# Optimization experiments

Hardware: AMD Instinct MI355X
Metric: run time of the kernel (lower is better)

The kernel has to match this reference:

```python
import jax, jax.numpy as jnp
import numpy as np

N_EXPERTS = 8
TOP_K = 2
C = 2048       # n_embd
H = 1024       # expert_intermediate_size
HS = 2048      # shared_expert_intermediate_size
B, T = 1, 512
SCALE = 0.02


def setup_inputs() -> dict:
    key = jax.random.key(0)
    ks = jax.random.split(key, 10)
    x = jax.random.normal(ks[0], (B, T, C), dtype=jnp.float32)
    gate_w = jax.random.normal(ks[1], (N_EXPERTS, C), dtype=jnp.float32) * SCALE
    w_gate = jax.random.normal(ks[2], (N_EXPERTS, H, C), dtype=jnp.float32) * SCALE
    w_up = jax.random.normal(ks[3], (N_EXPERTS, H, C), dtype=jnp.float32) * SCALE
    w_down = jax.random.normal(ks[4], (N_EXPERTS, C, H), dtype=jnp.float32) * SCALE
    sh_gate = jax.random.normal(ks[5], (HS, C), dtype=jnp.float32) * SCALE
    sh_up = jax.random.normal(ks[6], (HS, C), dtype=jnp.float32) * SCALE
    sh_down = jax.random.normal(ks[7], (C, HS), dtype=jnp.float32) * SCALE
    se_gate_w = jax.random.normal(ks[8], (1, C), dtype=jnp.float32) * SCALE
    return {"x": x, "gate_w": gate_w, "w_gate": w_gate, "w_up": w_up,
            "w_down": w_down, "sh_gate": sh_gate, "sh_up": sh_up,
            "sh_down": sh_down, "se_gate_w": se_gate_w}


def reference(x, gate_w, w_gate, w_up, w_down, sh_gate, sh_up, sh_down, se_gate_w):
    Bb, Tt, Cc = x.shape
    xf = x.reshape(-1, Cc)                      # (t, d)
    # routing
    scores = xf @ gate_w.T                      # (t, E)
    ew, ei = jax.lax.top_k(scores, TOP_K)       # (t, A)
    ew = jax.nn.softmax(ew, axis=-1)
    # expert FFN (dense over experts; identical math to per-token gathered einsum)
    x1 = jax.nn.silu(jnp.einsum('td,ehd->teh', xf, w_gate))
    x3 = jnp.einsum('td,ehd->teh', xf, w_up)
    expert_out = jnp.einsum('teh,edh->ted', x1 * x3, w_down)  # (t, E, d)
    # combine: routed[t] = sum_a ew[t,a] * expert_out[t, ei[t,a]]
    onehot = jax.nn.one_hot(ei, N_EXPERTS, dtype=ew.dtype)    # (t, A, E)
    comb = jnp.einsum('ta,tae->te', ew, onehot)               # (t, E)
    routed = jnp.einsum('te,ted->td', comb, expert_out)
    # shared expert (SwiGLU MLP)
    shared = (jax.nn.silu(xf @ sh_gate.T) * (xf @ sh_up.T)) @ sh_down.T
    sgate = jax.nn.sigmoid(xf @ se_gate_w.T)                  # (t, 1)
    return (routed + sgate * shared).reshape(Bb, Tt, Cc)
```

## Files before the change

### kernel.cpp

```cpp
#include <hip/hip_runtime.h>

typedef unsigned short u16;
typedef u16 u16x8 __attribute__((ext_vector_type(8)));
typedef __bf16 bf16x8 __attribute__((ext_vector_type(8)));
typedef float f32x4 __attribute__((ext_vector_type(4)));

#define NE 8

__device__ __forceinline__ unsigned pk2(float a, float b) {
  unsigned ua = __builtin_bit_cast(unsigned, a) + 0x8000u;
  unsigned ub = __builtin_bit_cast(unsigned, b) + 0x8000u;
  return __builtin_amdgcn_perm(ub, ua, 0x07060302);
}
__device__ __forceinline__ u16 f2bf(float f) {
  return (u16)((__builtin_bit_cast(unsigned, f) + 0x8000u) >> 16);
}
__device__ __forceinline__ bf16x8 ldfrag(const u16* p) {
  union { u16x8 u; bf16x8 b; } x;
  x.u = *(const u16x8*)p;
  return x.b;
}
__device__ __forceinline__ void gld16(const void* g, void* l) {
  __builtin_amdgcn_global_load_lds(
      (const __attribute__((address_space(1))) unsigned int*)g,
      (__attribute__((address_space(3))) unsigned int*)l, 16, 0, 0);
}
#define MFMA16 __builtin_amdgcn_mfma_f32_16x16x32_bf16

__global__ __launch_bounds__(64) void route_prep_kernel(
    const float* __restrict__ x, const float* __restrict__ gw,
    const float* __restrict__ segw, int* __restrict__ counts,
    int* __restrict__ ptok, float* __restrict__ pw, float* __restrict__ sgate,
    u16* __restrict__ xb) {
  int t = blockIdx.x;
  int lane = threadIdx.x;
  const float* xr = x + (size_t)t * 2048;
  u16* xbr = xb + (size_t)t * 2048;
  float s[NE];
#pragma unroll
  for (int e = 0; e < NE; e++) s[e] = 0.f;
  float sg = 0.f;
#pragma unroll
  for (int it = 0; it < 8; it++) {
    int c = it * 256 + lane * 4;
    f32x4 xv = *(const f32x4*)(xr + c);
    *(uint2*)(xbr + c) = make_uint2(pk2(xv[0], xv[1]), pk2(xv[2], xv[3]));
#pragma unroll
    for (int e = 0; e < NE; e++) {
      f32x4 wv4 = *(const f32x4*)(gw + e * 2048 + c);
      s[e] += xv[0] * wv4[0] + xv[1] * wv4[1] + xv[2] * wv4[2] + xv[3] * wv4[3];
    }
    f32x4 sv = *(const f32x4*)(segw + c);
    sg += xv[0] * sv[0] + xv[1] * sv[1] + xv[2] * sv[2] + xv[3] * sv[3];
  }
#pragma unroll
  for (int off = 32; off > 0; off >>= 1) {
#pragma unroll
    for (int e = 0; e < NE; e++) s[e] += __shfl_down(s[e], off);
    sg += __shfl_down(sg, off);
  }
  if (lane == 0) {
    int i0 = 0;
#pragma unroll
    for (int e = 1; e < NE; e++) if (s[e] > s[i0]) i0 = e;
    int i1 = (i0 == 0) ? 1 : 0;
#pragma unroll
    for (int e = 0; e < NE; e++) if (e != i0 && s[e] > s[i1]) i1 = e;
    float r = __expf(s[i1] - s[i0]);
    float w0 = 1.f / (1.f + r);
    float w1 = 1.f - w0;
    int s0 = atomicAdd(&counts[i0], 1);
    ptok[(i0 << 9) + s0] = t; pw[(i0 << 9) + s0] = w0;
    int s1 = atomicAdd(&counts[i1], 1);
    ptok[(i1 << 9) + s1] = t; pw[(i1 << 9) + s1] = w1;
    sgate[t] = 1.f / (1.f + __expf(-sg));
  }
}

__global__ __launch_bounds__(256) void gateup_kernel(
    const u16* __restrict__ xb, const float* __restrict__ Wg,
    const float* __restrict__ Wu, const float* __restrict__ SWg,
    const float* __restrict__ SWu, u16* __restrict__ hbufB,
    u16* __restrict__ hsB, const int* __restrict__ ptok,
    const int* __restrict__ counts) {
  __shared__ __align__(16) u16 As[3 * 8192];
  __shared__ __align__(16) u16 Bs[3 * 4096];

  int b = blockIdx.x;
  int t = threadIdx.x;
  int is_ex = (b < 1024);
  int e = 0, j, mt, cnt;
  const float *gW, *uW;
  u16* obase;
  if (is_ex) {
    e = b & 7; j = (b >> 3) & 31; mt = b >> 8;
    cnt = counts[e];
    if (mt * 128 >= cnt) return;
    gW = Wg + (size_t)(e * 1024 + j * 32) * 2048;
    uW = Wu + (size_t)(e * 1024 + j * 32) * 2048;
    obase = hbufB + (size_t)(e * 64 + 2 * j) * 8192;
  } else {
    int bs = b - 1024;
    int xcd = bs & 7; mt = (bs >> 3) & 3; j = (bs >> 5) * 8 + xcd; cnt = 512;
    gW = SWg + (size_t)(j * 32) * 2048;
    uW = SWu + (size_t)(j * 32) * 2048;
    obase = hsB + (size_t)(2 * j) * 8192;
  }

  int lane = t & 63, wv = t >> 6;
  int quad = lane >> 4, l16 = lane & 15;

  const u16* aptr[4];
  int aoff[4];
#pragma unroll
  for (int i = 0; i < 4; i++) {
    int c = 4 * wv + i;
    int row = 8 * c + (lane >> 3);
    int slot = mt * 128 + row;
    int tok = is_ex ? ((slot < cnt) ? ptok[(e << 9) + slot] : 0) : slot;
    aptr[i] = xb + (size_t)tok * 2048 + (((lane & 7) ^ ((lane >> 3) & 7)) * 8);
    aoff[i] = c * 512;
  }
  const float* bsrc[4];
  int bwr[4];
#pragma unroll
  for (int i = 0; i < 4; i++) {
    int rloc = wv * 16 + i * 4 + quad;
    const float* base = (rloc < 32) ? (gW + (size_t)rloc * 2048)
                                    : (uW + (size_t)(rloc - 32) * 2048);
    bsrc[i] = base + l16 * 4;
    bwr[i] = rloc * 64 + (((l16 >> 1) ^ (rloc & 7)) * 8) + ((l16 & 1) * 4);
  }

  f32x4 bA0, bA1, bA2, bA3, bB0, bB1, bB2, bB3;
  f32x4 acc00 = {}, acc01 = {}, acc02 = {}, acc03 = {};
  f32x4 acc10 = {}, acc11 = {}, acc12 = {}, acc13 = {};

#define GU_ISSUE(kt1, ao, S)                                                \
  S##0 = *(const f32x4*)(bsrc[0] + (kt1) * 64);                             \
  S##1 = *(const f32x4*)(bsrc[1] + (kt1) * 64);                             \
  S##2 = *(const f32x4*)(bsrc[2] + (kt1) * 64);                             \
  S##3 = *(const f32x4*)(bsrc[3] + (kt1) * 64);                             \
  gld16(aptr[0] + (kt1) * 64, &As[(ao) + aoff[0]]);                         \
  gld16(aptr[1] + (kt1) * 64, &As[(ao) + aoff[1]]);                         \
  gld16(aptr[2] + (kt1) * 64, &As[(ao) + aoff[2]]);                         \
  gld16(aptr[3] + (kt1) * 64, &As[(ao) + aoff[3]]);                         \
  __builtin_amdgcn_sched_barrier(0);

#define GU_WRITEB(ao, S)                                                    \
  *(uint2*)(&Bs[((ao) >> 1) + bwr[0]]) =                                    \
      make_uint2(pk2(S##0[0], S##0[1]), pk2(S##0[2], S##0[3]));             \
  *(uint2*)(&Bs[((ao) >> 1) + bwr[1]]) =                                    \
      make_uint2(pk2(S##1[0], S##1[1]), pk2(S##1[2], S##1[3]));             \
  *(uint2*)(&Bs[((ao) >> 1) + bwr[2]]) =                                    \
      make_uint2(pk2(S##2[0], S##2[1]), pk2(S##2[2], S##2[3]));             \
  *(uint2*)(&Bs[((ao) >> 1) + bwr[3]]) =                                    \
      make_uint2(pk2(S##3[0], S##3[1]), pk2(S##3[2], S##3[3]));

#define GU_COMPUTE(ao)                                                      \
  _Pragma("unroll") for (int k2 = 0; k2 < 2; k2++) {                        \
    int sl = ((k2 * 4 + quad) ^ (l16 & 7)) * 8;                             \
    bf16x8 af0 = ldfrag(&As[(ao) + (wv * 32 + l16) * 64 + sl]);             \
    bf16x8 af1 = ldfrag(&As[(ao) + (wv * 32 + 16 + l16) * 64 + sl]);        \
    bf16x8 bf0 = ldfrag(&Bs[((ao) >> 1) + l16 * 64 + sl]);                  \
    bf16x8 bf1 = ldfrag(&Bs[((ao) >> 1) + (16 + l16) * 64 + sl]);           \
    bf16x8 bf2 = ldfrag(&Bs[((ao) >> 1) + (32 + l16) * 64 + sl]);           \
    bf16x8 bf3 = ldfrag(&Bs[((ao) >> 1) + (48 + l16) * 64 + sl]);           \
    acc00 = MFMA16(af0, bf0, acc00, 0, 0, 0);                               \
    acc01 = MFMA16(af0, bf1, acc01, 0, 0, 0);                               \
    acc02 = MFMA16(af0, bf2, acc02, 0, 0, 0);                               \
    acc03 = MFMA16(af0, bf3, acc03, 0, 0, 0);                               \
    acc10 = MFMA16(af1, bf0, acc10, 0, 0, 0);                               \
    acc11 = MFMA16(af1, bf1, acc11, 0, 0, 0);                               \
    acc12 = MFMA16(af1, bf2, acc12, 0, 0, 0);                               \
    acc13 = MFMA16(af1, bf3, acc13, 0, 0, 0);                               \
  }

#define GU_PHASE(kt, aoC, aoI, aoW, Si, Sw)                                 \
  GU_ISSUE((kt) + 2, aoI, Si)                                               \
  GU_COMPUTE(aoC)                                                           \
  asm volatile("s_waitcnt vmcnt(8)" ::: "memory");                          \
  __builtin_amdgcn_sched_barrier(0);                                        \
  GU_WRITEB(aoW, Sw)                                                        \
  asm volatile("s_waitcnt lgkmcnt(0)" ::: "memory");                        \
  __builtin_amdgcn_s_barrier();                                             \
  __builtin_amdgcn_sched_barrier(0);

  int o0 = 0, o1 = 8192, o2 = 16384;
  GU_ISSUE(0, o0, bA)
  GU_ISSUE(1, o1, bB)
  asm volatile("s_waitcnt vmcnt(8)" ::: "memory");
  __builtin_amdgcn_sched_barrier(0);
  GU_WRITEB(o0, bA)
  asm volatile("s_waitcnt lgkmcnt(0)" ::: "memory");
  __builtin_amdgcn_s_barrier();
  __builtin_amdgcn_sched_barrier(0);

  for (int kt = 0; kt < 30; kt += 2) {
    GU_PHASE(kt, o0, o2, o1, bA, bB)
    GU_PHASE(kt + 1, o1, o0, o2, bB, bA)
    int tmp = o0; o0 = o2; o2 = o1; o1 = tmp;
  }
  GU_COMPUTE(o0)
  asm volatile("s_waitcnt vmcnt(0)" ::: "memory");
  __builtin_amdgcn_sched_barrier(0);
  GU_WRITEB(o1, bB)
  asm volatile("s_waitcnt lgkmcnt(0)" ::: "memory");
  __builtin_amdgcn_s_barrier();
  __builtin_amdgcn_sched_barrier(0);
  GU_COMPUTE(o1)
#undef GU_ISSUE
#undef GU_WRITEB
#undef GU_COMPUTE
#undef GU_PHASE

#define GU_EPI(AG, AU, i, n)                                                \
  _Pragma("unroll") for (int g = 0; g < 4; g++) {                           \
    int rloc = wv * 32 + (i) * 16 + quad * 4 + g;                           \
    int slot = mt * 128 + rloc;                                             \
    if (slot < cnt) {                                                       \
      float gv = AG[g], uv = AU[g];                                         \
      float h = gv / (1.f + __expf(-gv)) * uv;                              \
      obase[(size_t)(n) * 8192 + slot * 16 + l16] = f2bf(h);                \
    }                                                                       \
  }
  GU_EPI(acc00, acc02, 0, 0)
  GU_EPI(acc01, acc03, 0, 1)
  GU_EPI(acc10, acc12, 1, 0)
  GU_EPI(acc11, acc13, 1, 1)
#undef GU_EPI
}

__global__ __launch_bounds__(256) void down_kernel(
    const u16* __restrict__ hbufB, const u16* __restrict__ hsB,
    const float* __restrict__ Wd, const float* __restrict__ SWd,
    float* __restrict__ out, const int* __restrict__ ptok,
    const float* __restrict__ pw, const int* __restrict__ counts,
    const float* __restrict__ sgate) {
  __shared__ __align__(16) u16 As[3 * 8192];
  __shared__ __align__(16) u16 Bs[3 * 4096];

  int b = blockIdx.x;
  int t = threadIdx.x;
  int lane = t & 63, wv = t >> 6;
  int quad = lane >> 4, l16 = lane & 15;

#define DN_ISSUE(kt1, ao, S)                                                \
  S##0 = *(const f32x4*)(bsrc[0] + (kt1) * 64);                             \
  S##1 = *(const f32x4*)(bsrc[1] + (kt1) * 64);                             \
  S##2 = *(const f32x4*)(bsrc[2] + (kt1) * 64);                             \
  S##3 = *(const f32x4*)(bsrc[3] + (kt1) * 64);                             \
  gld16(aptr[0] + (size_t)(kt1) * 32768, &As[(ao) + aoff[0]]);              \
  gld16(aptr[1] + (size_t)(kt1) * 32768, &As[(ao) + aoff[1]]);              \
  gld16(aptr[2] + (size_t)(kt1) * 32768, &As[(ao) + aoff[2]]);              \
  gld16(aptr[3] + (size_t)(kt1) * 32768, &As[(ao) + aoff[3]]);              \
  __builtin_amdgcn_sched_barrier(0);

#define DN_WRITEB(ao, S)                                                    \
  *(uint2*)(&Bs[((ao) >> 1) + bwr[0]]) =                                    \
      make_uint2(pk2(S##0[0], S##0[1]), pk2(S##0[2], S##0[3]));             \
  *(uint2*)(&Bs[((ao) >> 1) + bwr[1]]) =                                    \
      make_uint2(pk2(S##1[0], S##1[1]), pk2(S##1[2], S##1[3]));             \
  *(uint2*)(&Bs[((ao) >> 1) + bwr[2]]) =                                    \
      make_uint2(pk2(S##2[0], S##2[1]), pk2(S##2[2], S##2[3]));             \
  *(uint2*)(&Bs[((ao) >> 1) + bwr[3]]) =                                    \
      make_uint2(pk2(S##3[0], S##3[1]), pk2(S##3[2], S##3[3]));

#define DN_COMPUTE(ao)                                                      \
  _Pragma("unroll") for (int k2 = 0; k2 < 2; k2++) {                        \
    int jsec = (k2 * 2 + (quad >> 1)) * 2048 +                              \
               (((quad & 1) ^ ((l16 >> 2) & 1)) * 8);                       \
    int sl = ((k2 * 4 + quad) ^ (l16 & 7)) * 8;                             \
    bf16x8 af0 = ldfrag(&As[(ao) + jsec + (wv * 32 + l16) * 16]);           \
    bf16x8 af1 = ldfrag(&As[(ao) + jsec + (wv * 32 + 16 + l16) * 16]);      \
    bf16x8 bf0 = ldfrag(&Bs[((ao) >> 1) + l16 * 64 + sl]);                  \
    bf16x8 bf1 = ldfrag(&Bs[((ao) >> 1) + (16 + l16) * 64 + sl]);           \
    bf16x8 bf2 = ldfrag(&Bs[((ao) >> 1) + (32 + l16) * 64 + sl]);           \
    bf16x8 bf3 = ldfrag(&Bs[((ao) >> 1) + (48 + l16) * 64 + sl]);           \
    acc00 = MFMA16(af0, bf0, acc00, 0, 0, 0);                               \
    acc01 = MFMA16(af0, bf1, acc01, 0, 0, 0);                               \
    acc02 = MFMA16(af0, bf2, acc02, 0, 0, 0);                               \
    acc03 = MFMA16(af0, bf3, acc03, 0, 0, 0);                               \
    acc10 = MFMA16(af1, bf0, acc10, 0, 0, 0);                               \
    acc11 = MFMA16(af1, bf1, acc11, 0, 0, 0);                               \
    acc12 = MFMA16(af1, bf2, acc12, 0, 0, 0);                               \
    acc13 = MFMA16(af1, bf3, acc13, 0, 0, 0);                               \
  }

#define DN_PHASE(kt, aoC, aoI, aoW, Si, Sw)                                 \
  DN_ISSUE((kt) + 2, aoI, Si)                                               \
  DN_COMPUTE(aoC)                                                           \
  asm volatile("s_waitcnt vmcnt(8)" ::: "memory");                          \
  __builtin_amdgcn_sched_barrier(0);                                        \
  DN_WRITEB(aoW, Sw)                                                        \
  asm volatile("s_waitcnt lgkmcnt(0)" ::: "memory");                        \
  __builtin_amdgcn_s_barrier();                                             \
  __builtin_amdgcn_sched_barrier(0);

#define DN_PROLOGUE                                                         \
  DN_ISSUE(0, o0, bA)                                                       \
  DN_ISSUE(1, o1, bB)                                                       \
  asm volatile("s_waitcnt vmcnt(8)" ::: "memory");                          \
  __builtin_amdgcn_sched_barrier(0);                                        \
  DN_WRITEB(o0, bA)                                                         \
  asm volatile("s_waitcnt lgkmcnt(0)" ::: "memory");                        \
  __builtin_amdgcn_s_barrier();                                             \
  __builtin_amdgcn_sched_barrier(0);

#define DN_TAIL                                                             \
  DN_COMPUTE(o0)                                                            \
  asm volatile("s_waitcnt vmcnt(0)" ::: "memory");                          \
  __builtin_amdgcn_sched_barrier(0);                                        \
  DN_WRITEB(o1, bB)                                                         \
  asm volatile("s_waitcnt lgkmcnt(0)" ::: "memory");                        \
  __builtin_amdgcn_s_barrier();                                             \
  __builtin_amdgcn_sched_barrier(0);                                        \
  DN_COMPUTE(o1)

  if (b < 1024) {
    int e = b & 7, nt = (b >> 3) & 31, mt = b >> 8;
    int cnt = counts[e];
    if (mt * 128 >= cnt) return;
    const u16* hb = hbufB + (size_t)e * 524288;

    const u16* aptr[4];
    int aoff[4];
#pragma unroll
    for (int i = 0; i < 4; i++) {
      aptr[i] = hb + (size_t)wv * 8192 +
                (size_t)(mt * 128 + i * 32 + (lane >> 1)) * 16 +
                (((lane & 1) ^ ((lane >> 3) & 1)) * 8);
      aoff[i] = wv * 2048 + i * 512;
    }
    const float* bsrc[4];
    int bwr[4];
#pragma unroll
    for (int i = 0; i < 4; i++) {
      int rloc = wv * 16 + i * 4 + quad;
      bsrc[i] = Wd + (size_t)(e * 2048 + nt * 64 + rloc) * 1024 + l16 * 4;
      bwr[i] = rloc * 64 + (((l16 >> 1) ^ (rloc & 7)) * 8) + ((l16 & 1) * 4);
    }

    f32x4 bA0, bA1, bA2, bA3, bB0, bB1, bB2, bB3;
    f32x4 acc00 = {}, acc01 = {}, acc02 = {}, acc03 = {};
    f32x4 acc10 = {}, acc11 = {}, acc12 = {}, acc13 = {};

    int o0 = 0, o1 = 8192, o2 = 16384;
    DN_PROLOGUE
    for (int kt = 0; kt < 14; kt += 2) {
      DN_PHASE(kt, o0, o2, o1, bA, bB)
      DN_PHASE(kt + 1, o1, o0, o2, bB, bA)
      int tmp = o0; o0 = o2; o2 = o1; o1 = tmp;
    }
    DN_TAIL

#define DE_EPI(ACC, i, n)                                                   \
  _Pragma("unroll") for (int g = 0; g < 4; g++) {                           \
    int sl = mt * 128 + wv * 32 + (i) * 16 + quad * 4 + g;                  \
    if (sl < cnt) {                                                         \
      atomicAdd(&out[(size_t)ptok[(e << 9) + sl] * 2048 + nt * 64 +         \
                     (n) * 16 + l16],                                       \
                pw[(e << 9) + sl] * ACC[g]);                                \
    }                                                                       \
  }
    DE_EPI(acc00, 0, 0) DE_EPI(acc01, 0, 1) DE_EPI(acc02, 0, 2) DE_EPI(acc03, 0, 3)
    DE_EPI(acc10, 1, 0) DE_EPI(acc11, 1, 1) DE_EPI(acc12, 1, 2) DE_EPI(acc13, 1, 3)
#undef DE_EPI
  } else {
    int bs = b - 1024;
    int xcd = bs & 7, mt = (bs >> 3) & 3, nt = (bs >> 5) * 8 + xcd;

    const u16* aptr[4];
    int aoff[4];
#pragma unroll
    for (int i = 0; i < 4; i++) {
      aptr[i] = hsB + (size_t)wv * 8192 +
                (size_t)(mt * 128 + i * 32 + (lane >> 1)) * 16 +
                (((lane & 1) ^ ((lane >> 3) & 1)) * 8);
      aoff[i] = wv * 2048 + i * 512;
    }
    const float* bsrc[4];
    int bwr[4];
#pragma unroll
    for (int i = 0; i < 4; i++) {
      int rloc = wv * 16 + i * 4 + quad;
      bsrc[i] = SWd + (size_t)(nt * 64 + rloc) * 2048 + l16 * 4;
      bwr[i] = rloc * 64 + (((l16 >> 1) ^ (rloc & 7)) * 8) + ((l16 & 1) * 4);
    }

    f32x4 bA0, bA1, bA2, bA3, bB0, bB1, bB2, bB3;
    f32x4 acc00 = {}, acc01 = {}, acc02 = {}, acc03 = {};
    f32x4 acc10 = {}, acc11 = {}, acc12 = {}, acc13 = {};

    int o0 = 0, o1 = 8192, o2 = 16384;
    DN_PROLOGUE
    for (int kt = 0; kt < 30; kt += 2) {
      DN_PHASE(kt, o0, o2, o1, bA, bB)
      DN_PHASE(kt + 1, o1, o0, o2, bB, bA)
      int tmp = o0; o0 = o2; o2 = o1; o1 = tmp;
    }
    DN_TAIL

#define DS_EPI(ACC, i, n)                                                   \
  _Pragma("unroll") for (int g = 0; g < 4; g++) {                           \
    int row = mt * 128 + wv * 32 + (i) * 16 + quad * 4 + g;                 \
    atomicAdd(&out[(size_t)row * 2048 + nt * 64 + (n) * 16 + l16],          \
              sgate[row] * ACC[g]);                                         \
  }
    DS_EPI(acc00, 0, 0) DS_EPI(acc01, 0, 1) DS_EPI(acc02, 0, 2) DS_EPI(acc03, 0, 3)
    DS_EPI(acc10, 1, 0) DS_EPI(acc11, 1, 1) DS_EPI(acc12, 1, 2) DS_EPI(acc13, 1, 3)
#undef DS_EPI
  }
#undef DN_ISSUE
#undef DN_WRITEB
#undef DN_COMPUTE
#undef DN_PHASE
#undef DN_PROLOGUE
#undef DN_TAIL
}

extern "C" void kernel_launch(void* const* d_in, const int* in_sizes, int n_in,
                              void* d_out, int out_size, void* d_ws, size_t ws_size,
                              hipStream_t stream) {
  const float* x = (const float*)d_in[0];
  const float* gate_w = (const float*)d_in[1];
  const float* w_gate = (const float*)d_in[2];
  const float* w_up = (const float*)d_in[3];
  const float* w_down = (const float*)d_in[4];
  const float* sh_gate = (const float*)d_in[5];
  const float* sh_up = (const float*)d_in[6];
  const float* sh_down = (const float*)d_in[7];
  const float* se_gate_w = (const float*)d_in[8];
  float* out = (float*)d_out;

  char* ws = (char*)d_ws;
  int* counts = (int*)(ws + 0);
  int* ptok = (int*)(ws + 1024);
  float* pw = (float*)(ws + 1024 + 16384);
  float* sg = (float*)(ws + 1024 + 32768);
  u16* xb = (u16*)(ws + 65536);
  u16* hbufB = (u16*)(ws + 65536 + (2u << 20));
  u16* hsB = (u16*)(ws + 65536 + (10u << 20));

  hipMemsetAsync(counts, 0, 32, stream);
  hipMemsetAsync(out, 0, out_size, stream);
  route_prep_kernel<<<512, 64, 0, stream>>>(x, gate_w, se_gate_w, counts,
                                            ptok, pw, sg, xb);
  gateup_kernel<<<1280, 256, 0, stream>>>(xb, w_gate, w_up, sh_gate, sh_up,
                                          hbufB, hsB, ptok, counts);
  down_kernel<<<1152, 256, 0, stream>>>(hbufB, hsB, w_down, sh_down, out,
                                        ptok, pw, counts, sg);
}
```

Baseline: 353.8 us.

## Switch GEMM pipelines to double buffering with per-block rotated K start

Both the gate/up and down GEMM kernels drop from a triple-buffered, two-stage-ahead prefetch to a double-buffered, one-stage-ahead loop. This cuts LDS use from 72KB to 48KB per block, which may allow more resident blocks. Each block also starts its K loop at a rotated offset derived from the block index, spreading concurrent weight reads across different K slices. The cost is shallower prefetch and a full vmcnt(0) wait before every barrier, which can expose more memory latency.

```diff
diff --git a/kernel.cpp b/kernel.cpp
--- a/kernel.cpp
+++ b/kernel.cpp
@@ -83,8 +83,8 @@
     const float* __restrict__ SWu, u16* __restrict__ hbufB,
     u16* __restrict__ hsB, const int* __restrict__ ptok,
     const int* __restrict__ counts) {
-  __shared__ __align__(16) u16 As[3 * 8192];
-  __shared__ __align__(16) u16 Bs[3 * 4096];
+  __shared__ __align__(16) u16 As[2 * 8192];
+  __shared__ __align__(16) u16 Bs[2 * 4096];
 
   int b = blockIdx.x;
   int t = threadIdx.x;
@@ -109,6 +109,7 @@
 
   int lane = t & 63, wv = t >> 6;
   int quad = lane >> 4, l16 = lane & 15;
+  int kt0 = (b * 11) & 31;
 
   const u16* aptr[4];
   int aoff[4];
@@ -132,30 +133,35 @@
     bwr[i] = rloc * 64 + (((l16 >> 1) ^ (rloc & 7)) * 8) + ((l16 & 1) * 4);
   }
 
-  f32x4 bA0, bA1, bA2, bA3, bB0, bB1, bB2, bB3;
+  f32x4 bv0, bv1, bv2, bv3;
   f32x4 acc00 = {}, acc01 = {}, acc02 = {}, acc03 = {};
   f32x4 acc10 = {}, acc11 = {}, acc12 = {}, acc13 = {};
 
-#define GU_ISSUE(kt1, ao, S)                                                \
-  S##0 = *(const f32x4*)(bsrc[0] + (kt1) * 64);                             \
-  S##1 = *(const f32x4*)(bsrc[1] + (kt1) * 64);                             \
-  S##2 = *(const f32x4*)(bsrc[2] + (kt1) * 64);                             \
-  S##3 = *(const f32x4*)(bsrc[3] + (kt1) * 64);                             \
-  gld16(aptr[0] + (kt1) * 64, &As[(ao) + aoff[0]]);                         \
-  gld16(aptr[1] + (kt1) * 64, &As[(ao) + aoff[1]]);                         \
-  gld16(aptr[2] + (kt1) * 64, &As[(ao) + aoff[2]]);                         \
-  gld16(aptr[3] + (kt1) * 64, &As[(ao) + aoff[3]]);                         \
+#define GU_ISSUE(kk, ao)                                                    \
+  bv0 = *(const f32x4*)(bsrc[0] + (kk) * 64);                               \
+  bv1 = *(const f32x4*)(bsrc[1] + (kk) * 64);                               \
+  bv2 = *(const f32x4*)(bsrc[2] + (kk) * 64);                               \
+  bv3 = *(const f32x4*)(bsrc[3] + (kk) * 64);                               \
+  gld16(aptr[0] + (kk) * 64, &As[(ao) + aoff[0]]);                          \
+  gld16(aptr[1] + (kk) * 64, &As[(ao) + aoff[1]]);                          \
+  gld16(aptr[2] + (kk) * 64, &As[(ao) + aoff[2]]);                          \
+  gld16(aptr[3] + (kk) * 64, &As[(ao) + aoff[3]]);                          \
   __builtin_amdgcn_sched_barrier(0);
 
-#define GU_WRITEB(ao, S)                                                    \
+#define GU_FINISH(ao)                                                       \
+  asm volatile("s_waitcnt vmcnt(4)" ::: "memory");                          \
+  __builtin_amdgcn_sched_barrier(0);                                        \
   *(uint2*)(&Bs[((ao) >> 1) + bwr[0]]) =                                    \
-      make_uint2(pk2(S##0[0], S##0[1]), pk2(S##0[2], S##0[3]));             \
+      make_uint2(pk2(bv0[0], bv0[1]), pk2(bv0[2], bv0[3]));                 \
   *(uint2*)(&Bs[((ao) >> 1) + bwr[1]]) =                                    \
-      make_uint2(pk2(S##1[0], S##1[1]), pk2(S##1[2], S##1[3]));             \
+      make_uint2(pk2(bv1[0], bv1[1]), pk2(bv1[2], bv1[3]));                 \
   *(uint2*)(&Bs[((ao) >> 1) + bwr[2]]) =                                    \
-      make_uint2(pk2(S##2[0], S##2[1]), pk2(S##2[2], S##2[3]));             \
+      make_uint2(pk2(bv2[0], bv2[1]), pk2(bv2[2], bv2[3]));                 \
   *(uint2*)(&Bs[((ao) >> 1) + bwr[3]]) =                                    \
-      make_uint2(pk2(S##3[0], S##3[1]), pk2(S##3[2], S##3[3]));
+      make_uint2(pk2(bv3[0], bv3[1]), pk2(bv3[2], bv3[3]));                 \
+  asm volatile("s_waitcnt vmcnt(0) lgkmcnt(0)" ::: "memory");               \
+  __builtin_amdgcn_s_barrier();                                             \
+  __builtin_amdgcn_sched_barrier(0);
 
 #define GU_COMPUTE(ao)                                                      \
   _Pragma("unroll") for (int k2 = 0; k2 < 2; k2++) {                        \
@@ -176,43 +182,17 @@
     acc13 = MFMA16(af1, bf3, acc13, 0, 0, 0);                               \
   }
 
-#define GU_PHASE(kt, aoC, aoI, aoW, Si, Sw)                                 \
-  GU_ISSUE((kt) + 2, aoI, Si)                                               \
-  GU_COMPUTE(aoC)                                                           \
-  asm volatile("s_waitcnt vmcnt(8)" ::: "memory");                          \
-  __builtin_amdgcn_sched_barrier(0);                                        \
-  GU_WRITEB(aoW, Sw)                                                        \
-  asm volatile("s_waitcnt lgkmcnt(0)" ::: "memory");                        \
-  __builtin_amdgcn_s_barrier();                                             \
-  __builtin_amdgcn_sched_barrier(0);
-
-  int o0 = 0, o1 = 8192, o2 = 16384;
-  GU_ISSUE(0, o0, bA)
-  GU_ISSUE(1, o1, bB)
-  asm volatile("s_waitcnt vmcnt(8)" ::: "memory");
-  __builtin_amdgcn_sched_barrier(0);
-  GU_WRITEB(o0, bA)
-  asm volatile("s_waitcnt lgkmcnt(0)" ::: "memory");
-  __builtin_amdgcn_s_barrier();
-  __builtin_amdgcn_sched_barrier(0);
-
-  for (int kt = 0; kt < 30; kt += 2) {
-    GU_PHASE(kt, o0, o2, o1, bA, bB)
-    GU_PHASE(kt + 1, o1, o0, o2, bB, bA)
-    int tmp = o0; o0 = o2; o2 = o1; o1 = tmp;
-  }
-  GU_COMPUTE(o0)
-  asm volatile("s_waitcnt vmcnt(0)" ::: "memory");
-  __builtin_amdgcn_sched_barrier(0);
-  GU_WRITEB(o1, bB)
-  asm volatile("s_waitcnt lgkmcnt(0)" ::: "memory");
-  __builtin_amdgcn_s_barrier();
-  __builtin_amdgcn_sched_barrier(0);
-  GU_COMPUTE(o1)
+  GU_ISSUE(kt0, 0);
+  GU_FINISH(0);
+  for (int kt = 0; kt < 32; kt++) {
+    int ao0 = (kt & 1) * 8192, ao1 = 8192 - ao0;
+    if (kt < 31) { GU_ISSUE((kt + 1 + kt0) & 31, ao1); }
+    GU_COMPUTE(ao0);
+    if (kt < 31) { GU_FINISH(ao1); }
+  }
 #undef GU_ISSUE
-#undef GU_WRITEB
+#undef GU_FINISH
 #undef GU_COMPUTE
-#undef GU_PHASE
 
 #define GU_EPI(AG, AU, i, n)                                                \
   _Pragma("unroll") for (int g = 0; g < 4; g++) {                           \
@@ -237,34 +217,43 @@
     float* __restrict__ out, const int* __restrict__ ptok,
     const float* __restrict__ pw, const int* __restrict__ counts,
     const float* __restrict__ sgate) {
-  __shared__ __align__(16) u16 As[3 * 8192];
-  __shared__ __align__(16) u16 Bs[3 * 4096];
+  __shared__ __align__(16) u16 As[2 * 8192];
+  __shared__ __align__(16) u16 Bs[2 * 4096];
 
   int b = blockIdx.x;
   int t = threadIdx.x;
   int lane = t & 63, wv = t >> 6;
   int quad = lane >> 4, l16 = lane & 15;
 
-#define DN_ISSUE(kt1, ao, S)                                                \
-  S##0 = *(const f32x4*)(bsrc[0] + (kt1) * 64);                             \
-  S##1 = *(const f32x4*)(bsrc[1] + (kt1) * 64);                             \
-  S##2 = *(const f32x4*)(bsrc[2] + (kt1) * 64);                             \
-  S##3 = *(const f32x4*)(bsrc[3] + (kt1) * 64);                             \
-  gld16(aptr[0] + (size_t)(kt1) * 32768, &As[(ao) + aoff[0]]);              \
-  gld16(aptr[1] + (size_t)(kt1) * 32768, &As[(ao) + aoff[1]]);              \
-  gld16(aptr[2] + (size_t)(kt1) * 32768, &As[(ao) + aoff[2]]);              \
-  gld16(aptr[3] + (size_t)(kt1) * 32768, &As[(ao) + aoff[3]]);              \
+  f32x4 bv0, bv1, bv2, bv3;
+  f32x4 acc00 = {}, acc01 = {}, acc02 = {}, acc03 = {};
+  f32x4 acc10 = {}, acc11 = {}, acc12 = {}, acc13 = {};
+
+#define DN_ISSUE(kk, ao)                                                    \
+  bv0 = *(const f32x4*)(bsrc[0] + (kk) * 64);                               \
+  bv1 = *(const f32x4*)(bsrc[1] + (kk) * 64);                               \
+  bv2 = *(const f32x4*)(bsrc[2] + (kk) * 64);                               \
+  bv3 = *(const f32x4*)(bsrc[3] + (kk) * 64);                               \
+  gld16(aptr[0] + (size_t)(kk) * 32768, &As[(ao) + aoff[0]]);               \
+  gld16(aptr[1] + (size_t)(kk) * 32768, &As[(ao) + aoff[1]]);               \
+  gld16(aptr[2] + (size_t)(kk) * 32768, &As[(ao) + aoff[2]]);               \
+  gld16(aptr[3] + (size_t)(kk) * 32768, &As[(ao) + aoff[3]]);               \
   __builtin_amdgcn_sched_barrier(0);
 
-#define DN_WRITEB(ao, S)                                                    \
+#define DN_FINISH(ao)                                                       \
+  asm volatile("s_waitcnt vmcnt(4)" ::: "memory");                          \
+  __builtin_amdgcn_sched_barrier(0);                                        \
   *(uint2*)(&Bs[((ao) >> 1) + bwr[0]]) =                                    \
-      make_uint2(pk2(S##0[0], S##0[1]), pk2(S##0[2], S##0[3]));             \
+      make_uint2(pk2(bv0[0], bv0[1]), pk2(bv0[2], bv0[3]));                 \
   *(uint2*)(&Bs[((ao) >> 1) + bwr[1]]) =                                    \
-      make_uint2(pk2(S##1[0], S##1[1]), pk2(S##1[2], S##1[3]));             \
+      make_uint2(pk2(bv1[0], bv1[1]), pk2(bv1[2], bv1[3]));                 \
   *(uint2*)(&Bs[((ao) >> 1) + bwr[2]]) =                                    \
-      make_uint2(pk2(S##2[0], S##2[1]), pk2(S##2[2], S##2[3]));             \
+      make_uint2(pk2(bv2[0], bv2[1]), pk2(bv2[2], bv2[3]));                 \
   *(uint2*)(&Bs[((ao) >> 1) + bwr[3]]) =                                    \
-      make_uint2(pk2(S##3[0], S##3[1]), pk2(S##3[2], S##3[3]));
+      make_uint2(pk2(bv3[0], bv3[1]), pk2(bv3[2], bv3[3]));                 \
+  asm volatile("s_waitcnt vmcnt(0) lgkmcnt(0)" ::: "memory");               \
+  __builtin_amdgcn_s_barrier();                                             \
+  __builtin_amdgcn_sched_barrier(0);
 
 #define DN_COMPUTE(ao)                                                      \
   _Pragma("unroll") for (int k2 = 0; k2 < 2; k2++) {                        \
@@ -287,41 +276,12 @@
     acc13 = MFMA16(af1, bf3, acc13, 0, 0, 0);                               \
   }
 
-#define DN_PHASE(kt, aoC, aoI, aoW, Si, Sw)                                 \
-  DN_ISSUE((kt) + 2, aoI, Si)                                               \
-  DN_COMPUTE(aoC)                                                           \
-  asm volatile("s_waitcnt vmcnt(8)" ::: "memory");                          \
-  __builtin_amdgcn_sched_barrier(0);                                        \
-  DN_WRITEB(aoW, Sw)                                                        \
-  asm volatile("s_waitcnt lgkmcnt(0)" ::: "memory");                        \
-  __builtin_amdgcn_s_barrier();                                             \
-  __builtin_amdgcn_sched_barrier(0);
-
-#define DN_PROLOGUE                                                         \
-  DN_ISSUE(0, o0, bA)                                                       \
-  DN_ISSUE(1, o1, bB)                                                       \
-  asm volatile("s_waitcnt vmcnt(8)" ::: "memory");                          \
-  __builtin_amdgcn_sched_barrier(0);                                        \
-  DN_WRITEB(o0, bA)                                                         \
-  asm volatile("s_waitcnt lgkmcnt(0)" ::: "memory");                        \
-  __builtin_amdgcn_s_barrier();                                             \
-  __builtin_amdgcn_sched_barrier(0);
-
-#define DN_TAIL                                                             \
-  DN_COMPUTE(o0)                                                            \
-  asm volatile("s_waitcnt vmcnt(0)" ::: "memory");                          \
-  __builtin_amdgcn_sched_barrier(0);                                        \
-  DN_WRITEB(o1, bB)                                                         \
-  asm volatile("s_waitcnt lgkmcnt(0)" ::: "memory");                        \
-  __builtin_amdgcn_s_barrier();                                             \
-  __builtin_amdgcn_sched_barrier(0);                                        \
-  DN_COMPUTE(o1)
-
   if (b < 1024) {
     int e = b & 7, nt = (b >> 3) & 31, mt = b >> 8;
     int cnt = counts[e];
     if (mt * 128 >= cnt) return;
     const u16* hb = hbufB + (size_t)e * 524288;
+    int kt0 = (b * 11) & 15;
 
     const u16* aptr[4];
     int aoff[4];
@@ -341,18 +301,14 @@
       bwr[i] = rloc * 64 + (((l16 >> 1) ^ (rloc & 7)) * 8) + ((l16 & 1) * 4);
     }
 
-    f32x4 bA0, bA1, bA2, bA3, bB0, bB1, bB2, bB3;
-    f32x4 acc00 = {}, acc01 = {}, acc02 = {}, acc03 = {};
-    f32x4 acc10 = {}, acc11 = {}, acc12 = {}, acc13 = {};
-
-    int o0 = 0, o1 = 8192, o2 = 16384;
-    DN_PROLOGUE
-    for (int kt = 0; kt < 14; kt += 2) {
-      DN_PHASE(kt, o0, o2, o1, bA, bB)
-      DN_PHASE(kt + 1, o1, o0, o2, bB, bA)
-      int tmp = o0; o0 = o2; o2 = o1; o1 = tmp;
-    }
-    DN_TAIL
+    DN_ISSUE(kt0, 0);
+    DN_FINISH(0);
+    for (int kt = 0; kt < 16; kt++) {
+      int ao0 = (kt & 1) * 8192, ao1 = 8192 - ao0;
+      if (kt < 15) { DN_ISSUE((kt + 1 + kt0) & 15, ao1); }
+      DN_COMPUTE(ao0);
+      if (kt < 15) { DN_FINISH(ao1); }
+    }
 
 #define DE_EPI(ACC, i, n)                                                   \
   _Pragma("unroll") for (int g = 0; g < 4; g++) {                           \
@@ -369,6 +325,7 @@
   } else {
     int bs = b - 1024;
     int xcd = bs & 7, mt = (bs >> 3) & 3, nt = (bs >> 5) * 8 + xcd;
+    int kt0 = (b * 11) & 31;
 
     const u16* aptr[4];
     int aoff[4];
@@ -388,18 +345,14 @@
       bwr[i] = rloc * 64 + (((l16 >> 1) ^ (rloc & 7)) * 8) + ((l16 & 1) * 4);
     }
 
-    f32x4 bA0, bA1, bA2, bA3, bB0, bB1, bB2, bB3;
-    f32x4 acc00 = {}, acc01 = {}, acc02 = {}, acc03 = {};
-    f32x4 acc10 = {}, acc11 = {}, acc12 = {}, acc13 = {};
-
-    int o0 = 0, o1 = 8192, o2 = 16384;
-    DN_PROLOGUE
-    for (int kt = 0; kt < 30; kt += 2) {
-      DN_PHASE(kt, o0, o2, o1, bA, bB)
-      DN_PHASE(kt + 1, o1, o0, o2, bB, bA)
-      int tmp = o0; o0 = o2; o2 = o1; o1 = tmp;
-    }
-    DN_TAIL
+    DN_ISSUE(kt0, 0);
+    DN_FINISH(0);
+    for (int kt = 0; kt < 32; kt++) {
+      int ao0 = (kt & 1) * 8192, ao1 = 8192 - ao0;
+      if (kt < 31) { DN_ISSUE((kt + 1 + kt0) & 31, ao1); }
+      DN_COMPUTE(ao0);
+      if (kt < 31) { DN_FINISH(ao1); }
+    }
 
 #define DS_EPI(ACC, i, n)                                                   \
   _Pragma("unroll") for (int g = 0; g < 4; g++) {                           \
@@ -412,11 +365,8 @@
 #undef DS_EPI
   }
 #undef DN_ISSUE
-#undef DN_WRITEB
+#undef DN_FINISH
 #undef DN_COMPUTE
-#undef DN_PHASE
-#undef DN_PROLOGUE
-#undef DN_TAIL
 }
 
 extern "C" void kernel_launch(void* const* d_in, const int* in_sizes, int n_in,
```

Result: faster. 315.4 us (-10.8%).
